# Performance work log

Hardware: AMD Instinct MI355X
Metric: run time of the kernel (lower is better)

Reference implementation:

```python
import jax, jax.numpy as jnp
import numpy as np

NEG_SLOPE = 0.1  # leaky_relu slope used by Conv1dNormRelu in the repo


def grid_sample_bilinear(feat, xy):
    """Bilinear sample feat [B,C,H,W] at pixel coords xy [B,2,N].

    Equivalent to the repo's grid_sample_wrapper: it normalizes xy to [-1,1]
    and calls F.grid_sample(align_corners=True, padding_mode='zeros'), which
    maps back to exactly these pixel coordinates. Out-of-bounds corners -> 0.
    Returns [B,C,N].
    """
    B, C, H, W = feat.shape
    x = xy[:, 0]  # [B,N]
    y = xy[:, 1]
    x0 = jnp.floor(x)
    y0 = jnp.floor(y)
    wx1 = x - x0
    wy1 = y - y0
    wx0 = 1.0 - wx1
    wy0 = 1.0 - wy1

    def gather(ix, iy):
        valid = (ix >= 0) & (ix <= W - 1) & (iy >= 0) & (iy <= H - 1)
        ixc = jnp.clip(ix, 0, W - 1).astype(jnp.int32)
        iyc = jnp.clip(iy, 0, H - 1).astype(jnp.int32)
        # per-batch gather: f[:, iy, ix] -> [C, N]
        v = jax.vmap(lambda f, iy_, ix_: f[:, iy_, ix_])(feat, iyc, ixc)  # [B,C,N]
        return v * valid[:, None, :].astype(feat.dtype)

    out = (gather(x0, y0) * (wx0 * wy0)[:, None, :]
           + gather(x0 + 1, y0) * (wx1 * wy0)[:, None, :]
           + gather(x0, y0 + 1) * (wx0 * wy1)[:, None, :]
           + gather(x0 + 1, y0 + 1) * (wx1 * wy1)[:, None, :])
    return out


def setup_inputs() -> dict:
    key = jax.random.key(0)
    k1, k2, k3, k4 = jax.random.split(key, 4)
    B, N = 4, 16384
    C2D, C3D, H, W_img = 128, 128, 96, 160
    # pixel coords in [0, W-1] x [0, H-1]
    u = jax.random.uniform(k1, (B, 1, N), dtype=jnp.float32) * (W_img - 1)
    v = jax.random.uniform(k2, (B, 1, N), dtype=jnp.float32) * (H - 1)
    xy = jnp.concatenate([u, v], axis=1)  # [B,2,N]
    feat_2d = jax.random.normal(k3, (B, C2D, H, W_img), dtype=jnp.float32)
    feat_3d = jax.random.normal(k4, (B, C3D, N), dtype=jnp.float32)
    kw, kb = jax.random.split(jax.random.fold_in(key, 7))
    fan_in = C2D + C3D
    W = jax.random.normal(kw, (C3D, fan_in), dtype=jnp.float32) / np.sqrt(fan_in)
    b = jnp.zeros((C3D,), dtype=jnp.float32)
    return {"xy": xy, "feat_2d": feat_2d, "feat_3d": feat_3d, "W": W, "b": b}


def reference(xy, feat_2d, feat_3d, W, b):
    # torch.no_grad() around the gather -> stop_gradient
    feat_2d_to_3d = jax.lax.stop_gradient(grid_sample_bilinear(feat_2d, xy))  # [B,C2d,N]
    cat = jnp.concatenate([feat_2d_to_3d, feat_3d], axis=1)  # [B,C2d+C3d,N]
    # Conv1d with kernel_size=1 == pointwise matmul over channels
    y = jnp.einsum('oi,bin->bon', W, cat) + b[None, :, None]
    return jnp.where(y >= 0, y, NEG_SLOPE * y)
```

## Files before the change

kernel.cpp:

```cpp
#include <hip/hip_runtime.h>
#include <hip/hip_bf16.h>

#define NSAMP 16384
#define BB    4
#define C2D   128
#define C3D   128
#define HH    96
#define WW    160
#define COUT  128
#define KK    256
#define TN    64
#define HW    (HH*WW)
#define CATS  264

typedef __attribute__((ext_vector_type(8))) short bf16x8;
typedef __attribute__((ext_vector_type(4))) float f32x4;

__device__ __forceinline__ float bf16lo(unsigned int u) { return __uint_as_float(u << 16); }
__device__ __forceinline__ float bf16hi(unsigned int u) { return __uint_as_float(u & 0xffff0000u); }
__device__ __forceinline__ unsigned int pack2(float a, float b) {
    union { __hip_bfloat162 h; unsigned int u; } c;
    c.h = __float22bfloat162_rn(make_float2(a, b));
    return c.u;
}

__global__ __launch_bounds__(256) void transpose_cvt_kernel(
    const float* __restrict__ f2d, unsigned short* __restrict__ f2dt)
{
    __shared__ unsigned short t[64 * 66];
    const int tid  = threadIdx.x;
    const int lane = tid & 63;
    const int wv   = tid >> 6;
    const int blk  = blockIdx.x;
    const int b    = blk / ((HW / 64) * 2);
    const int rem  = blk % ((HW / 64) * 2);
    const int c0   = (rem & 1) * 64;
    const int hw0  = (rem >> 1) * 64;

    #pragma unroll
    for (int s = 0; s < 16; ++s) {
        const int cl = s * 4 + wv;
        float v = f2d[(size_t)(b * C2D + c0 + cl) * HW + hw0 + lane];
        __hip_bfloat16 h = __float2bfloat16(v);
        t[lane * 66 + cl] = *(unsigned short*)&h;
    }
    __syncthreads();
    const unsigned int* tw  = (const unsigned int*)t;
    unsigned int*       wsu = (unsigned int*)f2dt;
    #pragma unroll
    for (int s = 0; s < 8; ++s) {
        const int hwl = s * 8 + (tid >> 5);
        const int cu  = tid & 31;
        wsu[((size_t)(b * HW + hw0 + hwl) * C2D + c0) / 2 + cu] = tw[hwl * 33 + cu];
    }
}

__global__ __launch_bounds__(256) void wcvt_kernel(
    const float* __restrict__ Wm, unsigned short* __restrict__ Wb)
{
    const int i = blockIdx.x * 256 + threadIdx.x;
    const float4 v = ((const float4*)Wm)[i];
    uint2 o;
    o.x = pack2(v.x, v.y);
    o.y = pack2(v.z, v.w);
    ((uint2*)Wb)[i] = o;
}

__global__ __launch_bounds__(256, 4) void fuse_kernel(
    const float*          __restrict__ xy,
    const unsigned short* __restrict__ f2dt,
    const float*          __restrict__ f3d,
    const unsigned short* __restrict__ Wb,
    const float*          __restrict__ bias,
    float* __restrict__ out)
{
    __shared__ unsigned short cat[TN * CATS];
    __shared__ float4 sw4[TN];
    __shared__ int4   soff4[TN];

    const int tid  = threadIdx.x;
    const int lane = tid & 63;
    const int wv   = tid >> 6;
    const int blk  = blockIdx.x;
    const int b    = blk >> 8;
    const int n0   = (blk & 255) * TN;

    if (tid < TN) {
        const int n = n0 + tid;
        float x = xy[((size_t)b * 2 + 0) * NSAMP + n];
        float y = xy[((size_t)b * 2 + 1) * NSAMP + n];
        float xf = floorf(x), yf = floorf(y);
        float wx1 = x - xf, wy1 = y - yf;
        float wx0 = 1.0f - wx1, wy0 = 1.0f - wy1;
        int x0 = (int)xf, y0 = (int)yf;
        int x1 = x0 + 1, y1 = y0 + 1;
        if (x0 < 0 || x0 > WW - 1) wx0 = 0.0f;
        if (x1 < 0 || x1 > WW - 1) wx1 = 0.0f;
        if (y0 < 0 || y0 > HH - 1) wy0 = 0.0f;
        if (y1 < 0 || y1 > HH - 1) wy1 = 0.0f;
        x0 = min(max(x0, 0), WW - 1);
        x1 = min(max(x1, 0), WW - 1);
        y0 = min(max(y0, 0), HH - 1);
        y1 = min(max(y1, 0), HH - 1);
        sw4[tid]   = make_float4(wx0 * wy0, wx1 * wy0, wx0 * wy1, wx1 * wy1);
        soff4[tid] = make_int4(y0 * WW + x0, y0 * WW + x1,
                               y1 * WW + x0, y1 * WW + x1);
    }
    __syncthreads();

    unsigned int* catw = (unsigned int*)cat;

    {
        const float* p3 = f3d + (size_t)(b * C3D) * NSAMP + n0 + lane;
        #pragma unroll
        for (int ch = 0; ch < 4; ++ch) {
            const int cbase = wv * 32 + ch * 8;
            float v[8];
            #pragma unroll
            for (int t = 0; t < 8; ++t) v[t] = p3[(size_t)(cbase + t) * NSAMP];
            uint4 pk;
            pk.x = pack2(v[0], v[1]);
            pk.y = pack2(v[2], v[3]);
            pk.z = pack2(v[4], v[5]);
            pk.w = pack2(v[6], v[7]);
            *(uint4*)&catw[lane * (CATS / 2) + (C2D / 2) + (cbase >> 1)] = pk;
        }
    }

    {
        const int s   = lane >> 5;
        const int ch4 = (lane & 31) * 4;
        const unsigned short* fb = f2dt + (size_t)b * HW * C2D + ch4;
        #pragma unroll 4
        for (int i = 0; i < 8; ++i) {
            const int j = wv * 16 + i * 2 + s;
            const float4 w = sw4[j];
            const int4   o = soff4[j];
            const uint2 c0v = *(const uint2*)(fb + (size_t)o.x * C2D);
            const uint2 c1v = *(const uint2*)(fb + (size_t)o.y * C2D);
            const uint2 c2v = *(const uint2*)(fb + (size_t)o.z * C2D);
            const uint2 c3v = *(const uint2*)(fb + (size_t)o.w * C2D);
            float r0 = w.x * bf16lo(c0v.x) + w.y * bf16lo(c1v.x)
                     + w.z * bf16lo(c2v.x) + w.w * bf16lo(c3v.x);
            float r1 = w.x * bf16hi(c0v.x) + w.y * bf16hi(c1v.x)
                     + w.z * bf16hi(c2v.x) + w.w * bf16hi(c3v.x);
            float r2 = w.x * bf16lo(c0v.y) + w.y * bf16lo(c1v.y)
                     + w.z * bf16lo(c2v.y) + w.w * bf16lo(c3v.y);
            float r3 = w.x * bf16hi(c0v.y) + w.y * bf16hi(c1v.y)
                     + w.z * bf16hi(c2v.y) + w.w * bf16hi(c3v.y);
            uint2 pk;
            pk.x = pack2(r0, r1);
            pk.y = pack2(r2, r3);
            *(uint2*)&catw[j * (CATS / 2) + (ch4 >> 1)] = pk;
        }
    }
    __syncthreads();

    {
        const int quad = lane >> 4;
        const int nloc = lane & 15;

        f32x4 acc[2][4];
        #pragma unroll
        for (int mt = 0; mt < 2; ++mt)
            #pragma unroll
            for (int nt = 0; nt < 4; ++nt)
                acc[mt][nt] = (f32x4){0.f, 0.f, 0.f, 0.f};

        const unsigned short* wb0 = Wb + (size_t)(wv * 32 + nloc) * KK + quad * 8;

        #pragma unroll 2
        for (int ks = 0; ks < 8; ++ks) {
            const int k0 = ks * 32;
            const bf16x8 a0 = *(const bf16x8*)(wb0 + k0);
            const bf16x8 a1 = *(const bf16x8*)(wb0 + 16 * KK + k0);
            #pragma unroll
            for (int nt = 0; nt < 4; ++nt) {
                const bf16x8 bfrag = *(const bf16x8*)
                    &cat[(nt * 16 + nloc) * CATS + k0 + quad * 8];
                acc[0][nt] = __builtin_amdgcn_mfma_f32_16x16x32_bf16(
                    a0, bfrag, acc[0][nt], 0, 0, 0);
                acc[1][nt] = __builtin_amdgcn_mfma_f32_16x16x32_bf16(
                    a1, bfrag, acc[1][nt], 0, 0, 0);
            }
        }

        #pragma unroll
        for (int mt = 0; mt < 2; ++mt) {
            const int cobase = wv * 32 + mt * 16 + quad * 4;
            float bv[4];
            #pragma unroll
            for (int r = 0; r < 4; ++r) bv[r] = bias[cobase + r];
            #pragma unroll
            for (int nt = 0; nt < 4; ++nt) {
                float* po = out + (size_t)(b * COUT + cobase) * NSAMP
                          + n0 + nt * 16 + nloc;
                #pragma unroll
                for (int r = 0; r < 4; ++r) {
                    float yv = acc[mt][nt][r] + bv[r];
                    yv = (yv >= 0.0f) ? yv : 0.1f * yv;
                    po[(size_t)r * NSAMP] = yv;
                }
            }
        }
    }
}

extern "C" void kernel_launch(void* const* d_in, const int* in_sizes, int n_in,
                              void* d_out, int out_size, void* d_ws, size_t ws_size,
                              hipStream_t stream) {
    const float* xy   = (const float*)d_in[0];
    const float* f2d  = (const float*)d_in[1];
    const float* f3d  = (const float*)d_in[2];
    const float* Wm   = (const float*)d_in[3];
    const float* bias = (const float*)d_in[4];
    float* out = (float*)d_out;

    unsigned short* f2dt = (unsigned short*)d_ws;
    unsigned short* Wb   = f2dt + (size_t)BB * HW * C2D;

    wcvt_kernel<<<dim3((COUT * KK / 4) / 256), 256, 0, stream>>>(Wm, Wb);
    transpose_cvt_kernel<<<dim3(BB * (HW / 64) * 2), 256, 0, stream>>>(f2d, f2dt);
    fuse_kernel<<<dim3(BB * (NSAMP / TN)), 256, 0, stream>>>(
        xy, f2dt, f3d, Wb, bias, out);
}
```

Measured before the change: 127.5 us.

## Apply 2D weight half before bilinear sampling and split the pointwise GEMM

Bilinear sampling is linear, so the 2D half of the 1x1 conv can be applied to the feature map before gathering. A new gemm1 kernel projects the full feat_2d grid through W's 2D half into a bf16 NHWC buffer G, and the fused kernel then gathers from G and only runs a K=128 MFMA for the 3D half. Shared-memory staging uses XOR swizzling in place of padding. The projection runs over H*W pixels (15360 per batch) instead of the 16384 samples, which trims per-sample MFMA work. It adds an extra bf16 rounding of the projected values before interpolation.

```diff
diff --git a/kernel.cpp b/kernel.cpp
--- a/kernel.cpp
+++ b/kernel.cpp
@@ -11,7 +11,6 @@
 #define KK    256
 #define TN    64
 #define HW    (HH*WW)
-#define CATS  264
 
 typedef __attribute__((ext_vector_type(8))) short bf16x8;
 typedef __attribute__((ext_vector_type(4))) float f32x4;
@@ -23,58 +22,117 @@
     c.h = __float22bfloat162_rn(make_float2(a, b));
     return c.u;
 }
-
-__global__ __launch_bounds__(256) void transpose_cvt_kernel(
-    const float* __restrict__ f2d, unsigned short* __restrict__ f2dt)
+#define SWZ(n, g) ((g) ^ ((n) & 7))
+
+__global__ __launch_bounds__(256) void wsplit_kernel(
+    const float* __restrict__ Wm,
+    unsigned short* __restrict__ Wb2, unsigned short* __restrict__ Wb3)
 {
-    __shared__ unsigned short t[64 * 66];
+    const int idx = blockIdx.x * 256 + threadIdx.x;
+    const float4 v = ((const float4*)Wm)[idx];
+    uint2 o;
+    o.x = pack2(v.x, v.y);
+    o.y = pack2(v.z, v.w);
+    const int row = idx >> 6;
+    const int c4  = idx & 63;
+    if (c4 < 32) ((uint2*)Wb2)[row * 32 + c4]        = o;
+    else         ((uint2*)Wb3)[row * 32 + (c4 - 32)] = o;
+}
+
+__global__ __launch_bounds__(256, 4) void gemm1_kernel(
+    const float*          __restrict__ f2d,
+    const unsigned short* __restrict__ Wb2,
+    unsigned short*       __restrict__ G)
+{
+    __shared__ unsigned short sB[64 * 128];
+    __shared__ unsigned short sO[64 * 136];
+
     const int tid  = threadIdx.x;
     const int lane = tid & 63;
     const int wv   = tid >> 6;
     const int blk  = blockIdx.x;
-    const int b    = blk / ((HW / 64) * 2);
-    const int rem  = blk % ((HW / 64) * 2);
-    const int c0   = (rem & 1) * 64;
-    const int hw0  = (rem >> 1) * 64;
-
+    const int b    = blk / (HW / 64);
+    const int hw0  = (blk % (HW / 64)) * 64;
+
+    {
+        const float* src = f2d + (size_t)(b * C2D + wv * 32) * HW + hw0 + lane;
+        unsigned int* sBw = (unsigned int*)sB;
+        #pragma unroll
+        for (int i = 0; i < 4; ++i) {
+            float v[8];
+            #pragma unroll
+            for (int j = 0; j < 8; ++j) v[j] = src[(size_t)(i * 8 + j) * HW];
+            uint4 pk;
+            pk.x = pack2(v[0], v[1]);
+            pk.y = pack2(v[2], v[3]);
+            pk.z = pack2(v[4], v[5]);
+            pk.w = pack2(v[6], v[7]);
+            const int g = wv * 4 + i;
+            *(uint4*)&sBw[lane * 64 + SWZ(lane, g) * 4] = pk;
+        }
+    }
+    __syncthreads();
+
+    const int quad = lane >> 4;
+    const int nloc = lane & 15;
+    f32x4 acc[2][4];
     #pragma unroll
-    for (int s = 0; s < 16; ++s) {
-        const int cl = s * 4 + wv;
-        float v = f2d[(size_t)(b * C2D + c0 + cl) * HW + hw0 + lane];
-        __hip_bfloat16 h = __float2bfloat16(v);
-        t[lane * 66 + cl] = *(unsigned short*)&h;
-    }
-    __syncthreads();
-    const unsigned int* tw  = (const unsigned int*)t;
-    unsigned int*       wsu = (unsigned int*)f2dt;
+    for (int mt = 0; mt < 2; ++mt)
+        #pragma unroll
+        for (int nt = 0; nt < 4; ++nt)
+            acc[mt][nt] = (f32x4){0.f, 0.f, 0.f, 0.f};
+
+    const unsigned short* wb0 = Wb2 + (size_t)(wv * 32 + nloc) * C2D + quad * 8;
     #pragma unroll
-    for (int s = 0; s < 8; ++s) {
-        const int hwl = s * 8 + (tid >> 5);
-        const int cu  = tid & 31;
-        wsu[((size_t)(b * HW + hw0 + hwl) * C2D + c0) / 2 + cu] = tw[hwl * 33 + cu];
-    }
-}
-
-__global__ __launch_bounds__(256) void wcvt_kernel(
-    const float* __restrict__ Wm, unsigned short* __restrict__ Wb)
-{
-    const int i = blockIdx.x * 256 + threadIdx.x;
-    const float4 v = ((const float4*)Wm)[i];
-    uint2 o;
-    o.x = pack2(v.x, v.y);
-    o.y = pack2(v.z, v.w);
-    ((uint2*)Wb)[i] = o;
-}
-
-__global__ __launch_bounds__(256, 4) void fuse_kernel(
+    for (int ks = 0; ks < 4; ++ks) {
+        const bf16x8 a0 = *(const bf16x8*)(wb0 + ks * 32);
+        const bf16x8 a1 = *(const bf16x8*)(wb0 + 16 * C2D + ks * 32);
+        #pragma unroll
+        for (int nt = 0; nt < 4; ++nt) {
+            const int n = nt * 16 + nloc;
+            const bf16x8 bf = *(const bf16x8*)
+                &sB[n * 128 + SWZ(n, ks * 4 + quad) * 8];
+            acc[0][nt] = __builtin_amdgcn_mfma_f32_16x16x32_bf16(a0, bf, acc[0][nt], 0, 0, 0);
+            acc[1][nt] = __builtin_amdgcn_mfma_f32_16x16x32_bf16(a1, bf, acc[1][nt], 0, 0, 0);
+        }
+    }
+
+    #pragma unroll
+    for (int mt = 0; mt < 2; ++mt) {
+        const int cobase = wv * 32 + mt * 16 + quad * 4;
+        #pragma unroll
+        for (int nt = 0; nt < 4; ++nt) {
+            const int n = nt * 16 + nloc;
+            uint2 pk;
+            pk.x = pack2(acc[mt][nt][0], acc[mt][nt][1]);
+            pk.y = pack2(acc[mt][nt][2], acc[mt][nt][3]);
+            *(uint2*)&sO[n * 136 + cobase] = pk;
+        }
+    }
+    __syncthreads();
+
+    {
+        unsigned int* Gw = (unsigned int*)(G + ((size_t)b * HW + hw0) * COUT);
+        const int q = tid & 15, r0 = tid >> 4;
+        #pragma unroll
+        for (int it = 0; it < 4; ++it) {
+            const int n = r0 + it * 16;
+            const uint4 v = *(const uint4*)&sO[n * 136 + q * 8];
+            *(uint4*)&Gw[n * 64 + q * 4] = v;
+        }
+    }
+}
+
+__global__ __launch_bounds__(256, 4) void fuse2_kernel(
     const float*          __restrict__ xy,
-    const unsigned short* __restrict__ f2dt,
+    const unsigned short* __restrict__ G,
     const float*          __restrict__ f3d,
-    const unsigned short* __restrict__ Wb,
+    const unsigned short* __restrict__ Wb3,
     const float*          __restrict__ bias,
     float* __restrict__ out)
 {
-    __shared__ unsigned short cat[TN * CATS];
+    __shared__ unsigned short sB[64 * 128];
+    __shared__ unsigned short g2[64 * 136];
     __shared__ float4 sw4[TN];
     __shared__ int4   soff4[TN];
 
@@ -108,38 +166,38 @@
     }
     __syncthreads();
 
-    unsigned int* catw = (unsigned int*)cat;
-
     {
         const float* p3 = f3d + (size_t)(b * C3D) * NSAMP + n0 + lane;
-        #pragma unroll
-        for (int ch = 0; ch < 4; ++ch) {
-            const int cbase = wv * 32 + ch * 8;
+        unsigned int* sBw = (unsigned int*)sB;
+        #pragma unroll
+        for (int i = 0; i < 4; ++i) {
+            const int cbase = wv * 32 + i * 8;
             float v[8];
             #pragma unroll
-            for (int t = 0; t < 8; ++t) v[t] = p3[(size_t)(cbase + t) * NSAMP];
+            for (int j = 0; j < 8; ++j) v[j] = p3[(size_t)(cbase + j) * NSAMP];
             uint4 pk;
             pk.x = pack2(v[0], v[1]);
             pk.y = pack2(v[2], v[3]);
             pk.z = pack2(v[4], v[5]);
             pk.w = pack2(v[6], v[7]);
-            *(uint4*)&catw[lane * (CATS / 2) + (C2D / 2) + (cbase >> 1)] = pk;
+            const int g = wv * 4 + i;
+            *(uint4*)&sBw[lane * 64 + SWZ(lane, g) * 4] = pk;
         }
     }
 
     {
         const int s   = lane >> 5;
         const int ch4 = (lane & 31) * 4;
-        const unsigned short* fb = f2dt + (size_t)b * HW * C2D + ch4;
+        const unsigned short* fb = G + (size_t)b * HW * COUT + ch4;
         #pragma unroll 4
         for (int i = 0; i < 8; ++i) {
             const int j = wv * 16 + i * 2 + s;
             const float4 w = sw4[j];
             const int4   o = soff4[j];
-            const uint2 c0v = *(const uint2*)(fb + (size_t)o.x * C2D);
-            const uint2 c1v = *(const uint2*)(fb + (size_t)o.y * C2D);
-            const uint2 c2v = *(const uint2*)(fb + (size_t)o.z * C2D);
-            const uint2 c3v = *(const uint2*)(fb + (size_t)o.w * C2D);
+            const uint2 c0v = *(const uint2*)(fb + (size_t)o.x * COUT);
+            const uint2 c1v = *(const uint2*)(fb + (size_t)o.y * COUT);
+            const uint2 c2v = *(const uint2*)(fb + (size_t)o.z * COUT);
+            const uint2 c3v = *(const uint2*)(fb + (size_t)o.w * COUT);
             float r0 = w.x * bf16lo(c0v.x) + w.y * bf16lo(c1v.x)
                      + w.z * bf16lo(c2v.x) + w.w * bf16lo(c3v.x);
             float r1 = w.x * bf16hi(c0v.x) + w.y * bf16hi(c1v.x)
@@ -151,7 +209,7 @@
             uint2 pk;
             pk.x = pack2(r0, r1);
             pk.y = pack2(r2, r3);
-            *(uint2*)&catw[j * (CATS / 2) + (ch4 >> 1)] = pk;
+            *(uint2*)&g2[j * 136 + ch4] = pk;
         }
     }
     __syncthreads();
@@ -167,37 +225,35 @@
             for (int nt = 0; nt < 4; ++nt)
                 acc[mt][nt] = (f32x4){0.f, 0.f, 0.f, 0.f};
 
-        const unsigned short* wb0 = Wb + (size_t)(wv * 32 + nloc) * KK + quad * 8;
-
-        #pragma unroll 2
-        for (int ks = 0; ks < 8; ++ks) {
-            const int k0 = ks * 32;
-            const bf16x8 a0 = *(const bf16x8*)(wb0 + k0);
-            const bf16x8 a1 = *(const bf16x8*)(wb0 + 16 * KK + k0);
+        const unsigned short* wb0 = Wb3 + (size_t)(wv * 32 + nloc) * C3D + quad * 8;
+        #pragma unroll
+        for (int ks = 0; ks < 4; ++ks) {
+            const bf16x8 a0 = *(const bf16x8*)(wb0 + ks * 32);
+            const bf16x8 a1 = *(const bf16x8*)(wb0 + 16 * C3D + ks * 32);
             #pragma unroll
             for (int nt = 0; nt < 4; ++nt) {
-                const bf16x8 bfrag = *(const bf16x8*)
-                    &cat[(nt * 16 + nloc) * CATS + k0 + quad * 8];
-                acc[0][nt] = __builtin_amdgcn_mfma_f32_16x16x32_bf16(
-                    a0, bfrag, acc[0][nt], 0, 0, 0);
-                acc[1][nt] = __builtin_amdgcn_mfma_f32_16x16x32_bf16(
-                    a1, bfrag, acc[1][nt], 0, 0, 0);
+                const int n = nt * 16 + nloc;
+                const bf16x8 bf = *(const bf16x8*)
+                    &sB[n * 128 + SWZ(n, ks * 4 + quad) * 8];
+                acc[0][nt] = __builtin_amdgcn_mfma_f32_16x16x32_bf16(a0, bf, acc[0][nt], 0, 0, 0);
+                acc[1][nt] = __builtin_amdgcn_mfma_f32_16x16x32_bf16(a1, bf, acc[1][nt], 0, 0, 0);
             }
         }
 
         #pragma unroll
         for (int mt = 0; mt < 2; ++mt) {
             const int cobase = wv * 32 + mt * 16 + quad * 4;
-            float bv[4];
-            #pragma unroll
-            for (int r = 0; r < 4; ++r) bv[r] = bias[cobase + r];
+            const float4 bv = *(const float4*)&bias[cobase];
             #pragma unroll
             for (int nt = 0; nt < 4; ++nt) {
-                float* po = out + (size_t)(b * COUT + cobase) * NSAMP
-                          + n0 + nt * 16 + nloc;
+                const int n = nt * 16 + nloc;
+                const uint2 gq = *(const uint2*)&g2[n * 136 + cobase];
+                float add[4] = { bf16lo(gq.x), bf16hi(gq.x),
+                                 bf16lo(gq.y), bf16hi(gq.y) };
+                float* po = out + (size_t)(b * COUT + cobase) * NSAMP + n0 + n;
                 #pragma unroll
                 for (int r = 0; r < 4; ++r) {
-                    float yv = acc[mt][nt][r] + bv[r];
+                    float yv = acc[mt][nt][r] + add[r] + ((const float*)&bv)[r];
                     yv = (yv >= 0.0f) ? yv : 0.1f * yv;
                     po[(size_t)r * NSAMP] = yv;
                 }
@@ -216,11 +272,12 @@
     const float* bias = (const float*)d_in[4];
     float* out = (float*)d_out;
 
-    unsigned short* f2dt = (unsigned short*)d_ws;
-    unsigned short* Wb   = f2dt + (size_t)BB * HW * C2D;
-
-    wcvt_kernel<<<dim3((COUT * KK / 4) / 256), 256, 0, stream>>>(Wm, Wb);
-    transpose_cvt_kernel<<<dim3(BB * (HW / 64) * 2), 256, 0, stream>>>(f2d, f2dt);
-    fuse_kernel<<<dim3(BB * (NSAMP / TN)), 256, 0, stream>>>(
-        xy, f2dt, f3d, Wb, bias, out);
-}
+    unsigned short* G   = (unsigned short*)d_ws;
+    unsigned short* Wb2 = G + (size_t)BB * HW * COUT;
+    unsigned short* Wb3 = Wb2 + (size_t)COUT * C2D;
+
+    wsplit_kernel<<<dim3(32), 256, 0, stream>>>(Wm, Wb2, Wb3);
+    gemm1_kernel<<<dim3(BB * (HW / 64)), 256, 0, stream>>>(f2d, Wb2, G);
+    fuse2_kernel<<<dim3(BB * (NSAMP / TN)), 256, 0, stream>>>(
+        xy, G, f3d, Wb3, bias, out);
+}
```

Result: no change. 129.7 us (+1.7%).
